# Kernel optimization log

Hardware: AMD Instinct MI355X
Metric: run time of the kernel (lower is better)

## Reference

```python
import jax, jax.numpy as jnp
import numpy as np

HIDDEN_DIM = 640
VOCAB_SIZE = 1024


def setup_inputs() -> dict:
    key = jax.random.key(0)
    kf, kp, kw, kb = jax.random.split(key, 4)
    B, T, U, H, V = 8, 256, 64, HIDDEN_DIM, VOCAB_SIZE
    f = jax.random.normal(kf, (B, T, H), dtype=jnp.float32)
    p = jax.random.normal(kp, (B, U, H), dtype=jnp.float32)
    # nn.Linear default init: U(-1/sqrt(H), 1/sqrt(H))
    bound = 1.0 / np.sqrt(H)
    W = jax.random.uniform(kw, (V, H), minval=-bound, maxval=bound, dtype=jnp.float32)
    b = jax.random.uniform(kb, (V,), minval=-bound, maxval=bound, dtype=jnp.float32)
    return {"f": f, "p": p, "W": W, "b": b}


def reference(f, p, W, b):
    # f: (B,T,H), p: (B,U,H) -> combined: (B,T,U,H)
    combined = f[:, :, None, :] + p[:, None, :, :]
    h = jax.nn.relu(combined)
    # Linear: h @ W^T + b -> (B,T,U,V)
    logits = jnp.einsum('btuh,vh->btuv', h, W) + b
    return logits
```

## Files before the change

### kernel.cpp

```cpp
#include <hip/hip_runtime.h>
#include <hip/hip_bf16.h>

#define BDIM 8
#define TDIM 256
#define UDIM 64
#define HDIM 640
#define VDIM 1024

#define MDIM (BDIM * TDIM * UDIM)

typedef __attribute__((ext_vector_type(8))) short short8;
typedef __attribute__((ext_vector_type(4))) float f32x4;

__device__ __forceinline__ ushort f2bf(float x) {
    union { float f; unsigned int u; } v; v.f = x;
    unsigned int r = (v.u + 0x7fffu + ((v.u >> 16) & 1u)) >> 16;
    return (ushort)r;
}

__global__ void cvt_w_kernel(const float* __restrict__ W, ushort* __restrict__ Wb) {
    int i = (blockIdx.x * 256 + threadIdx.x) * 4;
    f32x4 w = *(const f32x4*)(W + i);
    ushort4 o;
    o.x = f2bf(w[0]); o.y = f2bf(w[1]); o.z = f2bf(w[2]); o.w = f2bf(w[3]);
    *(ushort4*)(Wb + i) = o;
}

__global__ __launch_bounds__(256) void build_h_kernel(
    const float* __restrict__ f, const float* __restrict__ p,
    ushort* __restrict__ h)
{
    const int tid = threadIdx.x;
    const int row = (blockIdx.x << 5) + (tid >> 3);
    const int j0  = tid & 7;
    const int b = row >> 14;
    const int t = (row >> 6) & (TDIM - 1);
    const int u = row & (UDIM - 1);
    const float* frow = f + (size_t)(b * TDIM + t) * HDIM;
    const float* prow = p + (size_t)(b * UDIM + u) * HDIM;
    ushort* hrow = h + (size_t)row * HDIM;
    #pragma unroll
    for (int it = 0; it < HDIM / 64; ++it) {
        const int k = (j0 + it * 8) * 8;
        f32x4 f0 = *(const f32x4*)(frow + k);
        f32x4 f1 = *(const f32x4*)(frow + k + 4);
        f32x4 p0 = *(const f32x4*)(prow + k);
        f32x4 p1 = *(const f32x4*)(prow + k + 4);
        short8 hv;
        #pragma unroll
        for (int e = 0; e < 4; ++e) {
            float a0 = fmaxf(f0[e] + p0[e], 0.0f);
            float a1 = fmaxf(f1[e] + p1[e], 0.0f);
            hv[e]     = (short)f2bf(a0);
            hv[e + 4] = (short)f2bf(a1);
        }
        *(short8*)(hrow + k) = hv;
    }
}

__global__ __launch_bounds__(256) void hgemm_kernel(
    const ushort* __restrict__ h,
    const ushort* __restrict__ Wb,
    const float* __restrict__ bias,
    float* __restrict__ out)
{
    __shared__ ushort Alds[128 * 64];
    __shared__ ushort Blds[128 * 64];

    const int tid  = threadIdx.x;
    const int lane = tid & 63;
    const int wave = tid >> 6;
    const int wm   = wave >> 1;
    const int wn   = wave & 1;

    const int bid   = blockIdx.x;
    const int work  = (bid & 7) * 1024 + (bid >> 3);
    const int mtile = work >> 3;
    const int ntile = work & 7;
    const int m0 = mtile * 128;
    const int v0 = ntile * 128;

    const ushort* hbase  = h  + (size_t)m0 * HDIM;
    const ushort* wbbase = Wb + (size_t)v0 * HDIM;

    f32x4 acc[4][4];
    #pragma unroll
    for (int i = 0; i < 4; ++i)
        #pragma unroll
        for (int j = 0; j < 4; ++j)
            acc[i][j] = (f32x4)0.0f;

    for (int kt = 0; kt < HDIM / 64; ++kt) {
        const int k0 = kt * 64;
        __syncthreads();

        #pragma unroll
        for (int it = 0; it < 4; ++it) {
            const int c   = it * 256 + tid;
            const int row = c >> 3;
            const int j   = c & 7;
            const ushort* src = hbase + row * HDIM + k0 + ((j ^ (row & 7)) << 3);
            __builtin_amdgcn_global_load_lds(
                (const __attribute__((address_space(1))) void*)src,
                (__attribute__((address_space(3))) void*)(&Alds[(it * 256 + wave * 64) * 8]),
                16, 0, 0);
        }
        #pragma unroll
        for (int it = 0; it < 4; ++it) {
            const int c   = it * 256 + tid;
            const int row = c >> 3;
            const int j   = c & 7;
            const ushort* src = wbbase + row * HDIM + k0 + ((j ^ (row & 7)) << 3);
            __builtin_amdgcn_global_load_lds(
                (const __attribute__((address_space(1))) void*)src,
                (__attribute__((address_space(3))) void*)(&Blds[(it * 256 + wave * 64) * 8]),
                16, 0, 0);
        }

        __syncthreads();

        #pragma unroll
        for (int ks = 0; ks < 2; ++ks) {
            short8 afr[4], bfr[4];
            #pragma unroll
            for (int mi = 0; mi < 4; ++mi) {
                const int r = wm * 64 + mi * 16 + (lane & 15);
                const int j = ks * 4 + (lane >> 4);
                afr[mi] = *(const short8*)(&Alds[(r * 8 + (j ^ (r & 7))) * 8]);
            }
            #pragma unroll
            for (int ni = 0; ni < 4; ++ni) {
                const int r = wn * 64 + ni * 16 + (lane & 15);
                const int j = ks * 4 + (lane >> 4);
                bfr[ni] = *(const short8*)(&Blds[(r * 8 + (j ^ (r & 7))) * 8]);
            }
            #pragma unroll
            for (int mi = 0; mi < 4; ++mi)
                #pragma unroll
                for (int ni = 0; ni < 4; ++ni)
                    acc[mi][ni] = __builtin_amdgcn_mfma_f32_16x16x32_bf16(
                        afr[mi], bfr[ni], acc[mi][ni], 0, 0, 0);
        }
    }

    #pragma unroll
    for (int ni = 0; ni < 4; ++ni) {
        const int col = v0 + wn * 64 + ni * 16 + (lane & 15);
        const float bv = bias[col];
        #pragma unroll
        for (int mi = 0; mi < 4; ++mi) {
            const int rbase = m0 + wm * 64 + mi * 16 + ((lane >> 4) << 2);
            #pragma unroll
            for (int reg = 0; reg < 4; ++reg) {
                out[(size_t)(rbase + reg) * VDIM + col] = acc[mi][ni][reg] + bv;
            }
        }
    }
}

template <bool USE_WB>
__global__ __launch_bounds__(256) void joint_gemm_kernel(
    const float* __restrict__ f, const float* __restrict__ p,
    const float* __restrict__ Wf, const ushort* __restrict__ Wb,
    const float* __restrict__ bias, float* __restrict__ out)
{
    __shared__ ushort Alds[128 * 64];
    __shared__ ushort Blds[128 * 64];

    const int tid  = threadIdx.x;
    const int lane = tid & 63;
    const int wave = tid >> 6;
    const int wm   = wave >> 1;
    const int wn   = wave & 1;

    const int bid   = blockIdx.x;
    const int work  = (bid & 7) * 1024 + (bid >> 3);
    const int mtile = work >> 3;
    const int ntile = work & 7;
    const int m0 = mtile * 128;
    const int v0 = ntile * 128;

    const int b  = m0 >> 14;
    const int t0 = (m0 >> 6) & (TDIM - 1);

    const float*  fbase = f + (size_t)(b * TDIM + t0) * HDIM;
    const float*  pbase = p + (size_t)b * UDIM * HDIM;
    const ushort* wbbase = Wb + (size_t)v0 * HDIM;
    const float*  wfbase = Wf + (size_t)v0 * HDIM;

    f32x4 acc[4][4];
    #pragma unroll
    for (int i = 0; i < 4; ++i)
        #pragma unroll
        for (int j = 0; j < 4; ++j)
            acc[i][j] = (f32x4)0.0f;

    for (int kt = 0; kt < HDIM / 64; ++kt) {
        const int k0 = kt * 64;
        __syncthreads();

        if (USE_WB) {
            #pragma unroll
            for (int it = 0; it < 4; ++it) {
                const int c   = it * 256 + tid;
                const int row = c >> 3;
                const int j   = c & 7;
                const ushort* src = wbbase + row * HDIM + k0 + ((j ^ (row & 7)) << 3);
                __builtin_amdgcn_global_load_lds(
                    (const __attribute__((address_space(1))) void*)src,
                    (__attribute__((address_space(3))) void*)(&Blds[(it * 256 + wave * 64) * 8]),
                    16, 0, 0);
            }
        } else {
            #pragma unroll
            for (int it = 0; it < 4; ++it) {
                const int c   = it * 256 + tid;
                const int row = c >> 3;
                const int j   = c & 7;
                const float* wp = wfbase + row * HDIM + k0 + j * 8;
                f32x4 w0 = *(const f32x4*)wp;
                f32x4 w1 = *(const f32x4*)(wp + 4);
                short8 wv;
                #pragma unroll
                for (int e = 0; e < 4; ++e) {
                    wv[e]     = (short)f2bf(w0[e]);
                    wv[e + 4] = (short)f2bf(w1[e]);
                }
                *(short8*)(&Blds[(row * 8 + (j ^ (row & 7))) * 8]) = wv;
            }
        }

        #pragma unroll
        for (int it = 0; it < 4; ++it) {
            const int c   = it * 256 + tid;
            const int row = c >> 3;
            const int j   = c & 7;
            const float* fp_ = fbase + (row >> 6) * HDIM + k0 + j * 8;
            const float* pp_ = pbase + (row & 63) * HDIM + k0 + j * 8;
            f32x4 f0 = *(const f32x4*)fp_;
            f32x4 f1 = *(const f32x4*)(fp_ + 4);
            f32x4 p0 = *(const f32x4*)pp_;
            f32x4 p1 = *(const f32x4*)(pp_ + 4);
            short8 hv;
            #pragma unroll
            for (int e = 0; e < 4; ++e) {
                float a0 = fmaxf(f0[e] + p0[e], 0.0f);
                float a1 = fmaxf(f1[e] + p1[e], 0.0f);
                hv[e]     = (short)f2bf(a0);
                hv[e + 4] = (short)f2bf(a1);
            }
            *(short8*)(&Alds[(row * 8 + (j ^ (row & 7))) * 8]) = hv;
        }

        __syncthreads();

        #pragma unroll
        for (int ks = 0; ks < 2; ++ks) {
            short8 afr[4], bfr[4];
            #pragma unroll
            for (int mi = 0; mi < 4; ++mi) {
                const int r = wm * 64 + mi * 16 + (lane & 15);
                const int j = ks * 4 + (lane >> 4);
                afr[mi] = *(const short8*)(&Alds[(r * 8 + (j ^ (r & 7))) * 8]);
            }
            #pragma unroll
            for (int ni = 0; ni < 4; ++ni) {
                const int r = wn * 64 + ni * 16 + (lane & 15);
                const int j = ks * 4 + (lane >> 4);
                bfr[ni] = *(const short8*)(&Blds[(r * 8 + (j ^ (r & 7))) * 8]);
            }
            #pragma unroll
            for (int mi = 0; mi < 4; ++mi)
                #pragma unroll
                for (int ni = 0; ni < 4; ++ni)
                    acc[mi][ni] = __builtin_amdgcn_mfma_f32_16x16x32_bf16(
                        afr[mi], bfr[ni], acc[mi][ni], 0, 0, 0);
        }
    }

    #pragma unroll
    for (int ni = 0; ni < 4; ++ni) {
        const int col = v0 + wn * 64 + ni * 16 + (lane & 15);
        const float bv = bias[col];
        #pragma unroll
        for (int mi = 0; mi < 4; ++mi) {
            const int rbase = m0 + wm * 64 + mi * 16 + ((lane >> 4) << 2);
            #pragma unroll
            for (int reg = 0; reg < 4; ++reg) {
                out[(size_t)(rbase + reg) * VDIM + col] = acc[mi][ni][reg] + bv;
            }
        }
    }
}

extern "C" void kernel_launch(void* const* d_in, const int* in_sizes, int n_in,
                              void* d_out, int out_size, void* d_ws, size_t ws_size,
                              hipStream_t stream) {
    const float* f    = (const float*)d_in[0];
    const float* p    = (const float*)d_in[1];
    const float* W    = (const float*)d_in[2];
    const float* bias = (const float*)d_in[3];
    float* out = (float*)d_out;

    const int grid = (MDIM / 128) * (VDIM / 128);

    const size_t wb_bytes = (size_t)VDIM * HDIM * sizeof(ushort);
    const size_t h_bytes  = (size_t)MDIM * HDIM * sizeof(ushort);

    if (ws_size >= wb_bytes + h_bytes) {
        ushort* Wb = (ushort*)d_ws;
        ushort* h  = (ushort*)((char*)d_ws + wb_bytes);
        cvt_w_kernel<<<(VDIM * HDIM) / 1024, 256, 0, stream>>>(W, Wb);
        build_h_kernel<<<MDIM / 32, 256, 0, stream>>>(f, p, h);
        hgemm_kernel<<<grid, 256, 0, stream>>>(h, Wb, bias, out);
    } else if (ws_size >= wb_bytes) {
        ushort* Wb = (ushort*)d_ws;
        cvt_w_kernel<<<(VDIM * HDIM) / 1024, 256, 0, stream>>>(W, Wb);
        joint_gemm_kernel<true><<<grid, 256, 0, stream>>>(f, p, W, Wb, bias, out);
    } else {
        joint_gemm_kernel<false><<<grid, 256, 0, stream>>>(f, p, W, nullptr, bias, out);
    }
}
```

Baseline: 432.4 us.

## Use 256x256 tiles with double-buffered async LDS loads in hgemm

Replaces the 128x128 single-buffered GEMM with a 256x256 tile, 512-thread kernel whose K loop runs in 32-wide steps. Global-to-LDS loads for the next two K stages are issued ahead and waited on with explicit vmcnt counters, so memory traffic overlaps the MFMA work. Priority is raised around the MFMA section. Larger tiles raise arithmetic intensity and cut re-reads of h and W, at the cost of more registers per thread (128 accumulators), fewer blocks, and a changed LDS swizzle.

```diff
diff --git a/kernel.cpp b/kernel.cpp
--- a/kernel.cpp
+++ b/kernel.cpp
@@ -6,8 +6,12 @@
 #define UDIM 64
 #define HDIM 640
 #define VDIM 1024
-
 #define MDIM (BDIM * TDIM * UDIM)
+
+#define BM 256
+#define BN 256
+#define BK 32
+#define NT (HDIM / BK)
 
 typedef __attribute__((ext_vector_type(8))) short short8;
 typedef __attribute__((ext_vector_type(4))) float f32x4;
@@ -58,98 +62,119 @@
     }
 }
 
-__global__ __launch_bounds__(256) void hgemm_kernel(
+#define GLDS(srcptr, ldsptr)                                                   \
+    __builtin_amdgcn_global_load_lds(                                          \
+        (const __attribute__((address_space(1))) void*)(srcptr),               \
+        (__attribute__((address_space(3))) void*)(ldsptr), 16, 0, 0)
+
+__global__ __launch_bounds__(512) void hgemm256_kernel(
     const ushort* __restrict__ h,
     const ushort* __restrict__ Wb,
     const float* __restrict__ bias,
     float* __restrict__ out)
 {
-    __shared__ ushort Alds[128 * 64];
-    __shared__ ushort Blds[128 * 64];
+    __shared__ ushort Ash[2][BM * BK];
+    __shared__ ushort Bsh[2][BN * BK];
 
     const int tid  = threadIdx.x;
     const int lane = tid & 63;
     const int wave = tid >> 6;
-    const int wm   = wave >> 1;
-    const int wn   = wave & 1;
+    const int wm   = wave >> 2;
+    const int wn   = wave & 3;
 
     const int bid   = blockIdx.x;
-    const int work  = (bid & 7) * 1024 + (bid >> 3);
-    const int mtile = work >> 3;
-    const int ntile = work & 7;
-    const int m0 = mtile * 128;
-    const int v0 = ntile * 128;
-
-    const ushort* hbase  = h  + (size_t)m0 * HDIM;
-    const ushort* wbbase = Wb + (size_t)v0 * HDIM;
-
-    f32x4 acc[4][4];
-    #pragma unroll
-    for (int i = 0; i < 4; ++i)
+    const int work  = (bid & 7) * 256 + (bid >> 3);
+    const int mtile = work >> 2;
+    const int ntile = work & 3;
+    const int m0 = mtile * BM;
+    const int v0 = ntile * BN;
+
+    const ushort* hbase = h  + (size_t)m0 * HDIM;
+    const ushort* wbase = Wb + (size_t)v0 * HDIM;
+
+    const int row0 = tid >> 2;
+    const int j0   = tid & 3;
+    const int jg0  = j0 ^ ((row0 >> 1) & 3);
+    const size_t soff0 = (size_t)row0 * HDIM + jg0 * 8;
+    const size_t soff1 = soff0 + (size_t)128 * HDIM;
+    const int u0 = wave * 512;
+    const int u1 = 4096 + wave * 512;
+
+    int aoff[8], boff[4];
+    #pragma unroll
+    for (int mi = 0; mi < 8; ++mi) {
+        const int r = wm * 128 + mi * 16 + (lane & 15);
+        aoff[mi] = (r * 4 + ((lane >> 4) ^ ((r >> 1) & 3))) * 8;
+    }
+    #pragma unroll
+    for (int ni = 0; ni < 4; ++ni) {
+        const int r = wn * 64 + ni * 16 + (lane & 15);
+        boff[ni] = (r * 4 + ((lane >> 4) ^ ((r >> 1) & 3))) * 8;
+    }
+
+    f32x4 acc[8][4];
+    #pragma unroll
+    for (int i = 0; i < 8; ++i)
         #pragma unroll
         for (int j = 0; j < 4; ++j)
             acc[i][j] = (f32x4)0.0f;
 
-    for (int kt = 0; kt < HDIM / 64; ++kt) {
-        const int k0 = kt * 64;
-        __syncthreads();
-
-        #pragma unroll
-        for (int it = 0; it < 4; ++it) {
-            const int c   = it * 256 + tid;
-            const int row = c >> 3;
-            const int j   = c & 7;
-            const ushort* src = hbase + row * HDIM + k0 + ((j ^ (row & 7)) << 3);
-            __builtin_amdgcn_global_load_lds(
-                (const __attribute__((address_space(1))) void*)src,
-                (__attribute__((address_space(3))) void*)(&Alds[(it * 256 + wave * 64) * 8]),
-                16, 0, 0);
-        }
-        #pragma unroll
-        for (int it = 0; it < 4; ++it) {
-            const int c   = it * 256 + tid;
-            const int row = c >> 3;
-            const int j   = c & 7;
-            const ushort* src = wbbase + row * HDIM + k0 + ((j ^ (row & 7)) << 3);
-            __builtin_amdgcn_global_load_lds(
-                (const __attribute__((address_space(1))) void*)src,
-                (__attribute__((address_space(3))) void*)(&Blds[(it * 256 + wave * 64) * 8]),
-                16, 0, 0);
-        }
-
-        __syncthreads();
-
-        #pragma unroll
-        for (int ks = 0; ks < 2; ++ks) {
-            short8 afr[4], bfr[4];
-            #pragma unroll
-            for (int mi = 0; mi < 4; ++mi) {
-                const int r = wm * 64 + mi * 16 + (lane & 15);
-                const int j = ks * 4 + (lane >> 4);
-                afr[mi] = *(const short8*)(&Alds[(r * 8 + (j ^ (r & 7))) * 8]);
-            }
-            #pragma unroll
-            for (int ni = 0; ni < 4; ++ni) {
-                const int r = wn * 64 + ni * 16 + (lane & 15);
-                const int j = ks * 4 + (lane >> 4);
-                bfr[ni] = *(const short8*)(&Blds[(r * 8 + (j ^ (r & 7))) * 8]);
-            }
-            #pragma unroll
-            for (int mi = 0; mi < 4; ++mi)
-                #pragma unroll
-                for (int ni = 0; ni < 4; ++ni)
-                    acc[mi][ni] = __builtin_amdgcn_mfma_f32_16x16x32_bf16(
-                        afr[mi], bfr[ni], acc[mi][ni], 0, 0, 0);
-        }
-    }
+#define STAGE(kt, bf) do {                                                     \
+        GLDS(hbase + soff0 + (kt) * BK, &Ash[bf][u0]);                         \
+        GLDS(hbase + soff1 + (kt) * BK, &Ash[bf][u1]);                         \
+        GLDS(wbase + soff0 + (kt) * BK, &Bsh[bf][u0]);                         \
+        GLDS(wbase + soff1 + (kt) * BK, &Bsh[bf][u1]);                         \
+    } while (0)
+
+    STAGE(0, 0);
+    STAGE(1, 1);
+
+    for (int kt = 0; kt < NT; ++kt) {
+        const int bf = kt & 1;
+        if (kt + 1 < NT) {
+            asm volatile("s_waitcnt vmcnt(4)" ::: "memory");
+        } else {
+            asm volatile("s_waitcnt vmcnt(0)" ::: "memory");
+        }
+        __builtin_amdgcn_sched_barrier(0);
+        __builtin_amdgcn_s_barrier();
+        __builtin_amdgcn_sched_barrier(0);
+
+        const ushort* Ab = &Ash[bf][0];
+        const ushort* Bb = &Bsh[bf][0];
+
+        short8 bfr[4];
+        #pragma unroll
+        for (int ni = 0; ni < 4; ++ni)
+            bfr[ni] = *(const short8*)(Bb + boff[ni]);
+
+        __builtin_amdgcn_s_setprio(1);
+        #pragma unroll
+        for (int mi = 0; mi < 8; ++mi) {
+            short8 av = *(const short8*)(Ab + aoff[mi]);
+            #pragma unroll
+            for (int ni = 0; ni < 4; ++ni)
+                acc[mi][ni] = __builtin_amdgcn_mfma_f32_16x16x32_bf16(
+                    av, bfr[ni], acc[mi][ni], 0, 0, 0);
+        }
+        __builtin_amdgcn_s_setprio(0);
+
+        asm volatile("s_waitcnt lgkmcnt(0)" ::: "memory");
+        __builtin_amdgcn_sched_barrier(0);
+        __builtin_amdgcn_s_barrier();
+        __builtin_amdgcn_sched_barrier(0);
+
+        if (kt + 2 < NT) STAGE(kt + 2, bf);
+    }
+#undef STAGE
 
     #pragma unroll
     for (int ni = 0; ni < 4; ++ni) {
         const int col = v0 + wn * 64 + ni * 16 + (lane & 15);
         const float bv = bias[col];
         #pragma unroll
-        for (int mi = 0; mi < 4; ++mi) {
-            const int rbase = m0 + wm * 64 + mi * 16 + ((lane >> 4) << 2);
+        for (int mi = 0; mi < 8; ++mi) {
+            const int rbase = m0 + wm * 128 + mi * 16 + ((lane >> 4) << 2);
             #pragma unroll
             for (int reg = 0; reg < 4; ++reg) {
                 out[(size_t)(rbase + reg) * VDIM + col] = acc[mi][ni][reg] + bv;
@@ -206,10 +231,7 @@
                 const int row = c >> 3;
                 const int j   = c & 7;
                 const ushort* src = wbbase + row * HDIM + k0 + ((j ^ (row & 7)) << 3);
-                __builtin_amdgcn_global_load_lds(
-                    (const __attribute__((address_space(1))) void*)src,
-                    (__attribute__((address_space(3))) void*)(&Blds[(it * 256 + wave * 64) * 8]),
-                    16, 0, 0);
+                GLDS(src, &Blds[(it * 256 + wave * 64) * 8]);
             }
         } else {
             #pragma unroll
@@ -302,8 +324,6 @@
     const float* bias = (const float*)d_in[3];
     float* out = (float*)d_out;
 
-    const int grid = (MDIM / 128) * (VDIM / 128);
-
     const size_t wb_bytes = (size_t)VDIM * HDIM * sizeof(ushort);
     const size_t h_bytes  = (size_t)MDIM * HDIM * sizeof(ushort);
 
@@ -312,12 +332,15 @@
         ushort* h  = (ushort*)((char*)d_ws + wb_bytes);
         cvt_w_kernel<<<(VDIM * HDIM) / 1024, 256, 0, stream>>>(W, Wb);
         build_h_kernel<<<MDIM / 32, 256, 0, stream>>>(f, p, h);
-        hgemm_kernel<<<grid, 256, 0, stream>>>(h, Wb, bias, out);
+        const int grid = (MDIM / BM) * (VDIM / BN);
+        hgemm256_kernel<<<grid, 512, 0, stream>>>(h, Wb, bias, out);
     } else if (ws_size >= wb_bytes) {
         ushort* Wb = (ushort*)d_ws;
         cvt_w_kernel<<<(VDIM * HDIM) / 1024, 256, 0, stream>>>(W, Wb);
-        joint_gemm_kernel<true><<<grid, 256, 0, stream>>>(f, p, W, Wb, bias, out);
+        joint_gemm_kernel<true><<<(MDIM / 128) * (VDIM / 128), 256, 0, stream>>>(
+            f, p, W, Wb, bias, out);
     } else {
-        joint_gemm_kernel<false><<<grid, 256, 0, stream>>>(f, p, W, nullptr, bias, out);
-    }
-}
+        joint_gemm_kernel<false><<<(MDIM / 128) * (VDIM / 128), 256, 0, stream>>>(
+            f, p, W, nullptr, bias, out);
+    }
+}
```

Measured after the change: 409.1 us. 1.06x faster.
